# Performance work log

Hardware: AMD Instinct MI355X
Metric: run time of the kernel (lower is better)

## Reference

```python
import jax, jax.numpy as jnp
import numpy as np

N = 200000
B = 1024          # batch_size (number of graphs/segments)
D = 256           # in_channels
STEPS = 3         # processing_steps


def setup_inputs() -> dict:
    key = jax.random.key(0)
    ks = jax.random.split(key, 6)
    x = jax.random.normal(ks[0], (N, D), dtype=jnp.float32)
    bank_kg = jnp.zeros((1,), dtype=jnp.float32)  # unused by forward
    batch = jnp.sort(jax.random.randint(ks[1], (N,), 0, B, dtype=jnp.int32))
    q_star = jax.random.normal(ks[2], (B, 2 * D), dtype=jnp.float32)
    s = 1.0 / np.sqrt(D)  # PyTorch LSTM init scale
    W_ih = jax.random.uniform(ks[3], (4 * D, 2 * D), jnp.float32, -s, s)
    W_hh = jax.random.uniform(ks[4], (4 * D, D), jnp.float32, -s, s)
    b_ih = jnp.zeros((4 * D,), dtype=jnp.float32)
    b_hh = jnp.zeros((4 * D,), dtype=jnp.float32)
    return {"x": x, "bank_kg": bank_kg, "batch": batch, "q_star": q_star,
            "W_ih": W_ih, "W_hh": W_hh, "b_ih": b_ih, "b_hh": b_hh}


def _lstm_cell(inp, h, c, W_ih, W_hh, b_ih, b_hh):
    # PyTorch gate order: i, f, g, o
    gates = inp @ W_ih.T + b_ih + h @ W_hh.T + b_hh  # [B, 4D]
    i, f, g, o = jnp.split(gates, 4, axis=-1)
    i = jax.nn.sigmoid(i)
    f = jax.nn.sigmoid(f)
    g = jnp.tanh(g)
    o = jax.nn.sigmoid(o)
    c = f * c + i * g
    h = o * jnp.tanh(c)
    return h, c


def _segment_softmax(e, batch, num_segments):
    # numerically stable softmax over nodes grouped by segment id
    emax = jax.ops.segment_max(e, batch, num_segments=num_segments)
    emax = jnp.where(jnp.isfinite(emax), emax, 0.0)  # guard empty segments
    ee = jnp.exp(e - emax[batch])
    denom = jax.ops.segment_sum(ee, batch, num_segments=num_segments)
    return ee / (denom[batch] + 1e-16)


def reference(x, bank_kg, batch, q_star, W_ih, W_hh, b_ih, b_hh):
    del bank_kg  # unused in the original forward
    h = jnp.zeros((B, D), dtype=x.dtype)
    c = jnp.zeros((B, D), dtype=x.dtype)
    for _ in range(STEPS):
        h, c = _lstm_cell(q_star, h, c, W_ih, W_hh, b_ih, b_hh)
        q = h                                       # [B, D]
        e = jnp.sum(x * q[batch], axis=-1)          # [N] attention logits
        a = _segment_softmax(e, batch, B)           # [N]
        r = jax.ops.segment_sum(a[:, None] * x, batch, num_segments=B)  # [B, D]
        q_star = jnp.concatenate([q, r], axis=-1)   # [B, 2D]
    return q_star
```

## Files before the change

kernel.cpp:

```cpp
#include <hip/hip_runtime.h>
#include <hip/hip_bf16.h>
#include <cstdint>


#define NN     200000
#define BSEG   1024
#define DD     256
#define KA     512
#define FOURD  1024

using bf16x8 = __attribute__((ext_vector_type(8))) __bf16;
using f32x4  = __attribute__((ext_vector_type(4))) float;

__device__ __forceinline__ float bf2f(unsigned int u) {
  union { unsigned int i; float f; } v; v.i = (u & 0xffffu) << 16; return v.f;
}
__device__ __forceinline__ unsigned short f2bf(float f) {
  union { float f; unsigned int i; } v; v.f = f;
  unsigned int x = v.i;
  if ((x & 0x7fffffffu) > 0x7f800000u) return (unsigned short)((x >> 16) | 0x40);
  return (unsigned short)((x + 0x7fffu + ((x >> 16) & 1u)) >> 16);
}
__device__ __forceinline__ void split_bf(float f, unsigned short& hi, unsigned short& lo) {
  hi = f2bf(f);
  lo = f2bf(f - bf2f(hi));
}

__global__ void prep_all(const int* __restrict__ batch, int* __restrict__ segs,
                         const float* __restrict__ Wih, const float* __restrict__ Whh,
                         const float* __restrict__ bih, const float* __restrict__ bhh,
                         unsigned short* __restrict__ W1hi, unsigned short* __restrict__ W1lo,
                         unsigned short* __restrict__ W2hi, unsigned short* __restrict__ W2lo,
                         float* __restrict__ bias,
                         const float* __restrict__ qst,
                         unsigned short* __restrict__ Ahi, unsigned short* __restrict__ Alo,
                         float* __restrict__ c) {
  int idx = blockIdx.x * 256 + threadIdx.x;
  if (idx <= BSEG) {
    int lo = 0, hi = NN;
    while (lo < hi) { int mid = (lo + hi) >> 1; if (batch[mid] < idx) lo = mid + 1; else hi = mid; }
    segs[idx] = lo;
  }
  if (idx < FOURD) bias[idx] = bih[idx] + bhh[idx];
  if (idx < FOURD * KA) {
    int j = idx / KA, k = idx - j * KA;
    float w1 = Wih[j * 512 + k];
    float w2 = (k < 256) ? (Wih[j * 512 + k] + Whh[j * 256 + k])
                         : Wih[j * 512 + k];
    unsigned short hi, lo;
    split_bf(w1, hi, lo); W1hi[idx] = hi; W1lo[idx] = lo;
    split_bf(w2, hi, lo); W2hi[idx] = hi; W2lo[idx] = lo;
  }
  if (idx < BSEG * KA) {
    unsigned short hi, lo; split_bf(qst[idx], hi, lo);
    Ahi[idx] = hi; Alo[idx] = lo;
  }
  if (idx < BSEG * DD) c[idx] = 0.f;
}

__global__ __launch_bounds__(256) void gemm_gates(const unsigned short* __restrict__ Ahi,
                                                  const unsigned short* __restrict__ Alo,
                                                  const unsigned short* __restrict__ Whi,
                                                  const unsigned short* __restrict__ Wlo,
                                                  float* __restrict__ gates) {
  int bx = blockIdx.x;
  int m0 = (bx >> 5) << 7;
  int n0 = (bx & 31) << 5;
  int t = threadIdx.x, w = t >> 6, lane = t & 63;
  int r16 = lane & 15, quad = lane >> 4;

  __shared__ unsigned short sWhi[32 * 64];
  __shared__ unsigned short sWlo[32 * 64];

  f32x4 acc[2][2] = {};

  const unsigned short* a0h = Ahi + (size_t)(m0 + 32 * w + r16) * KA + quad * 8;
  const unsigned short* a0l = Alo + (size_t)(m0 + 32 * w + r16) * KA + quad * 8;

  int srow = t >> 3;
  int scb  = t & 7;
  const unsigned short* gwh = Whi + (size_t)(n0 + srow) * KA + scb * 8;
  const unsigned short* gwl = Wlo + (size_t)(n0 + srow) * KA + scb * 8;
  int sdst = srow * 64 + ((scb ^ (srow & 7)) * 8);

  for (int kc = 0; kc < KA; kc += 64) {
    __syncthreads();
    *(bf16x8*)&sWhi[sdst] = *(const bf16x8*)(gwh + kc);
    *(bf16x8*)&sWlo[sdst] = *(const bf16x8*)(gwl + kc);
    __syncthreads();
    #pragma unroll
    for (int ks = 0; ks < 2; ++ks) {
      bf16x8 bh[2], bl[2];
      #pragma unroll
      for (int ni = 0; ni < 2; ++ni) {
        int wr = 16 * ni + r16;
        int off = wr * 64 + (((ks * 4 + quad) ^ (wr & 7)) * 8);
        bh[ni] = *(const bf16x8*)&sWhi[off];
        bl[ni] = *(const bf16x8*)&sWlo[off];
      }
      #pragma unroll
      for (int ms = 0; ms < 2; ++ms) {
        bf16x8 a  = *(const bf16x8*)(a0h + (size_t)ms * 16 * KA + kc + ks * 32);
        bf16x8 al = *(const bf16x8*)(a0l + (size_t)ms * 16 * KA + kc + ks * 32);
        #pragma unroll
        for (int ni = 0; ni < 2; ++ni) {
          acc[ms][ni] = __builtin_amdgcn_mfma_f32_16x16x32_bf16(a,  bh[ni], acc[ms][ni], 0, 0, 0);
          acc[ms][ni] = __builtin_amdgcn_mfma_f32_16x16x32_bf16(a,  bl[ni], acc[ms][ni], 0, 0, 0);
          acc[ms][ni] = __builtin_amdgcn_mfma_f32_16x16x32_bf16(al, bh[ni], acc[ms][ni], 0, 0, 0);
        }
      }
    }
  }
  #pragma unroll
  for (int ms = 0; ms < 2; ++ms)
    #pragma unroll
    for (int ni = 0; ni < 2; ++ni)
      #pragma unroll
      for (int r = 0; r < 4; ++r)
        gates[(size_t)(m0 + 32 * w + 16 * ms + quad * 4 + r) * FOURD
              + n0 + 16 * ni + r16] = acc[ms][ni][r];
}

#define LD1(dst, kk, base, RR) do {                                         \
    int i_ = w + 4 * (kk);                                                  \
    int ic_ = i_ < (RR) ? i_ : (RR) - 1;                                    \
    if (ic_ < 0) ic_ = 0;                                                   \
    int row_ = (base) + ic_;                                                \
    if (row_ > NN - 1) row_ = NN - 1;                                       \
    dst = *(const float4*)(x + (size_t)row_ * DD + lane * 4);               \
  } while (0)

#define ST1(src, kk) do {                                                   \
    int i_ = w + 4 * (kk);                                                  \
    if (i_ < R) *(float4*)&xt[i_ * DD + ((4 * lane) ^ (4 * (i_ & 7)))] = src; \
  } while (0)

#define LDALL(base, RR) do {                                                \
    LD1(st0, 0, base, RR); LD1(st1, 1, base, RR);                           \
    LD1(st2, 2, base, RR); LD1(st3, 3, base, RR);                           \
    LD1(st4, 4, base, RR); LD1(st5, 5, base, RR);                           \
    LD1(st6, 6, base, RR); LD1(st7, 7, base, RR);                           \
  } while (0)

#define STALL() do {                                                        \
    ST1(st0, 0); ST1(st1, 1); ST1(st2, 2); ST1(st3, 3);                     \
    ST1(st4, 4); ST1(st5, 5); ST1(st6, 6); ST1(st7, 7);                     \
  } while (0)

__global__ __launch_bounds__(256, 4) void attn_fused(const float* __restrict__ x,
                                                     const int* __restrict__ segs,
                                                     const float* __restrict__ gates,
                                                     const float* __restrict__ bias,
                                                     float* __restrict__ c,
                                                     unsigned short* __restrict__ Ahi,
                                                     unsigned short* __restrict__ Alo,
                                                     float* __restrict__ qout) {
  int b = blockIdx.x, t = threadIdx.x;
  int w = t >> 6, lane = t & 63;

  const float* g = gates + (size_t)b * FOURD;
  float gi = g[t]       + bias[t];
  float gf = g[256 + t] + bias[256 + t];
  float gg = g[512 + t] + bias[512 + t];
  float go = g[768 + t] + bias[768 + t];
  float ig = 1.f / (1.f + expf(-gi));
  float fg = 1.f / (1.f + expf(-gf));
  float gt = tanhf(gg);
  float og = 1.f / (1.f + expf(-go));
  int cidx = b * DD + t;
  float cn = fg * c[cidx] + ig * gt;
  c[cidx] = cn;
  float hn = og * tanhf(cn);

  __shared__ float shq[DD];
  __shared__ __align__(16) float xt[32 * DD];
  __shared__ float se[32];
  __shared__ float sm[4], sl[4];
  __shared__ __align__(16) float sv[4][DD];

  shq[t ^ (4 * ((t >> 5) & 7))] = hn;
  {
    unsigned short hi, lo; split_bf(hn, hi, lo);
    size_t ro = (size_t)b * KA;
    Ahi[ro + t] = hi;  Alo[ro + t] = lo;
    qout[(size_t)b * 512 + t] = hn;
  }
  __syncthreads();

  int s = segs[b], e = segs[b + 1];
  int r8 = lane >> 3, d8 = lane & 7;

  float m = -3.402823466e38f, l = 0.f;
  float4 v = {0.f, 0.f, 0.f, 0.f};

  int R = e - s; if (R > 32) R = 32;
  float4 st0, st1, st2, st3, st4, st5, st6, st7;
  LDALL(s, R);

  for (int tb = s; tb < e; tb += 32) {
    __syncthreads();
    STALL();
    __syncthreads();

    int base2 = tb + 32;
    int Rn = e - base2; if (Rn > 32) Rn = 32;
    LDALL(base2, Rn);

    {
      int i = 8 * w + r8;
      int key = 4 * (i & 7);
      float4 acc = {0.f, 0.f, 0.f, 0.f};
      #pragma unroll
      for (int cc = 0; cc < 8; ++cc) {
        int j = d8 * 32 + 4 * cc;
        float4 xv = *(const float4*)&xt[i * DD + (j ^ key)];
        float4 qv = *(const float4*)&shq[j ^ (4 * d8)];
        acc.x += xv.x * qv.x; acc.y += xv.y * qv.y;
        acc.z += xv.z * qv.z; acc.w += xv.w * qv.w;
      }
      float ee = (acc.x + acc.y) + (acc.z + acc.w);
      ee += __shfl_xor(ee, 1);
      ee += __shfl_xor(ee, 2);
      ee += __shfl_xor(ee, 4);
      if (i >= R) ee = -3.402823466e38f;
      if (d8 == 0) se[i] = ee;
    }
    __syncthreads();

    float tm = se[lane & 31];
    #pragma unroll
    for (int mask = 16; mask; mask >>= 1) tm = fmaxf(tm, __shfl_xor(tm, mask));
    float mn = fmaxf(m, tm);
    float alpha = __expf(m - mn);
    l *= alpha; v.x *= alpha; v.y *= alpha; v.z *= alpha; v.w *= alpha;

    #pragma unroll
    for (int k = 0; k < 8; ++k) {
      int i = w + 4 * k;
      if (i < R) {
        float wv = __expf(se[i] - mn);
        float4 xv = *(const float4*)&xt[i * DD + ((4 * lane) ^ (4 * (i & 7)))];
        l += wv;
        v.x += wv * xv.x; v.y += wv * xv.y; v.z += wv * xv.z; v.w += wv * xv.w;
      }
    }
    m = mn;
    R = Rn;
  }

  if (lane == 0) { sm[w] = m; sl[w] = l; }
  *(float4*)(&sv[w][lane * 4]) = v;
  __syncthreads();

  float M = fmaxf(fmaxf(sm[0], sm[1]), fmaxf(sm[2], sm[3]));
  if (M < -1e37f) M = 0.f;
  float a0 = __expf(sm[0] - M), a1 = __expf(sm[1] - M);
  float a2 = __expf(sm[2] - M), a3 = __expf(sm[3] - M);
  float L = sl[0] * a0 + sl[1] * a1 + sl[2] * a2 + sl[3] * a3;
  float r = (sv[0][t] * a0 + sv[1][t] * a1 + sv[2][t] * a2 + sv[3][t] * a3)
            / (L + 1e-16f);

  unsigned short hi, lo; split_bf(r, hi, lo);
  size_t ro = (size_t)b * KA;
  Ahi[ro + DD + t] = hi;  Alo[ro + DD + t] = lo;
  qout[(size_t)b * 512 + DD + t] = r;
}

extern "C" void kernel_launch(void* const* d_in, const int* in_sizes, int n_in,
                              void* d_out, int out_size, void* d_ws, size_t ws_size,
                              hipStream_t stream) {
  const float* x    = (const float*)d_in[0];
  const int*   batc = (const int*)d_in[2];
  const float* qst  = (const float*)d_in[3];
  const float* Wih  = (const float*)d_in[4];
  const float* Whh  = (const float*)d_in[5];
  const float* bih  = (const float*)d_in[6];
  const float* bhh  = (const float*)d_in[7];
  float* out = (float*)d_out;

  char* ws = (char*)d_ws;
  size_t off = 0;
  auto alloc = [&](size_t bytes) -> void* {
    void* p = ws + off; off = (off + bytes + 255) & ~(size_t)255; return p;
  };
  int*            segs = (int*)alloc((size_t)(BSEG + 1) * 4);
  unsigned short* W1hi = (unsigned short*)alloc((size_t)FOURD * KA * 2);
  unsigned short* W1lo = (unsigned short*)alloc((size_t)FOURD * KA * 2);
  unsigned short* W2hi = (unsigned short*)alloc((size_t)FOURD * KA * 2);
  unsigned short* W2lo = (unsigned short*)alloc((size_t)FOURD * KA * 2);
  unsigned short* Ahi  = (unsigned short*)alloc((size_t)BSEG * KA * 2);
  unsigned short* Alo  = (unsigned short*)alloc((size_t)BSEG * KA * 2);
  float*          gate = (float*)alloc((size_t)BSEG * FOURD * 4);
  float*          c    = (float*)alloc((size_t)BSEG * DD * 4);
  float*          bias = (float*)alloc((size_t)FOURD * 4);

  prep_all<<<(FOURD * KA + 255) / 256, 256, 0, stream>>>(
      batc, segs, Wih, Whh, bih, bhh, W1hi, W1lo, W2hi, W2lo, bias, qst, Ahi, Alo, c);

  for (int step = 0; step < 3; ++step) {
    const unsigned short* whi = step ? W2hi : W1hi;
    const unsigned short* wlo = step ? W2lo : W1lo;
    gemm_gates<<<256, 256, 0, stream>>>(Ahi, Alo, whi, wlo, gate);
    attn_fused<<<BSEG, 256, 0, stream>>>(x, segs, gate, bias, c, Ahi, Alo, out);
  }
}
```

Measured before the change: 428.9 us.

## Fuse prep, gate GEMM and attention into one persistent kernel with grid barriers

Replaces the prep kernel and the three gemm/attention launch pairs with a single 1024-block kernel that synchronises steps through a software grid barrier built on atomics. The LSTM cell state now stays in a register across steps, and the gate GEMM becomes a per-block 32x32 tile that reads operands directly from global memory with no LDS staging. The intent is to remove launch overhead and the round trips of c and bias through memory. In exchange, it requires all 1024 blocks to be co-resident (launch_bounds of 4 blocks per CU), which risks deadlock or spin overhead, and the GEMM loses its LDS reuse of the weights.

New measurement: 1.568 ms. 266% more time.

```diff
diff --git a/kernel.cpp b/kernel.cpp
--- a/kernel.cpp
+++ b/kernel.cpp
@@ -8,6 +8,7 @@
 #define DD     256
 #define KA     512
 #define FOURD  1024
+#define NBLK   1024
 
 using bf16x8 = __attribute__((ext_vector_type(8))) __bf16;
 using f32x4  = __attribute__((ext_vector_type(4))) float;
@@ -26,99 +27,24 @@
   lo = f2bf(f - bf2f(hi));
 }
 
-__global__ void prep_all(const int* __restrict__ batch, int* __restrict__ segs,
-                         const float* __restrict__ Wih, const float* __restrict__ Whh,
-                         const float* __restrict__ bih, const float* __restrict__ bhh,
-                         unsigned short* __restrict__ W1hi, unsigned short* __restrict__ W1lo,
-                         unsigned short* __restrict__ W2hi, unsigned short* __restrict__ W2lo,
-                         float* __restrict__ bias,
-                         const float* __restrict__ qst,
-                         unsigned short* __restrict__ Ahi, unsigned short* __restrict__ Alo,
-                         float* __restrict__ c) {
-  int idx = blockIdx.x * 256 + threadIdx.x;
-  if (idx <= BSEG) {
-    int lo = 0, hi = NN;
-    while (lo < hi) { int mid = (lo + hi) >> 1; if (batch[mid] < idx) lo = mid + 1; else hi = mid; }
-    segs[idx] = lo;
-  }
-  if (idx < FOURD) bias[idx] = bih[idx] + bhh[idx];
-  if (idx < FOURD * KA) {
-    int j = idx / KA, k = idx - j * KA;
-    float w1 = Wih[j * 512 + k];
-    float w2 = (k < 256) ? (Wih[j * 512 + k] + Whh[j * 256 + k])
-                         : Wih[j * 512 + k];
-    unsigned short hi, lo;
-    split_bf(w1, hi, lo); W1hi[idx] = hi; W1lo[idx] = lo;
-    split_bf(w2, hi, lo); W2hi[idx] = hi; W2lo[idx] = lo;
-  }
-  if (idx < BSEG * KA) {
-    unsigned short hi, lo; split_bf(qst[idx], hi, lo);
-    Ahi[idx] = hi; Alo[idx] = lo;
-  }
-  if (idx < BSEG * DD) c[idx] = 0.f;
-}
-
-__global__ __launch_bounds__(256) void gemm_gates(const unsigned short* __restrict__ Ahi,
-                                                  const unsigned short* __restrict__ Alo,
-                                                  const unsigned short* __restrict__ Whi,
-                                                  const unsigned short* __restrict__ Wlo,
-                                                  float* __restrict__ gates) {
-  int bx = blockIdx.x;
-  int m0 = (bx >> 5) << 7;
-  int n0 = (bx & 31) << 5;
-  int t = threadIdx.x, w = t >> 6, lane = t & 63;
-  int r16 = lane & 15, quad = lane >> 4;
-
-  __shared__ unsigned short sWhi[32 * 64];
-  __shared__ unsigned short sWlo[32 * 64];
-
-  f32x4 acc[2][2] = {};
-
-  const unsigned short* a0h = Ahi + (size_t)(m0 + 32 * w + r16) * KA + quad * 8;
-  const unsigned short* a0l = Alo + (size_t)(m0 + 32 * w + r16) * KA + quad * 8;
-
-  int srow = t >> 3;
-  int scb  = t & 7;
-  const unsigned short* gwh = Whi + (size_t)(n0 + srow) * KA + scb * 8;
-  const unsigned short* gwl = Wlo + (size_t)(n0 + srow) * KA + scb * 8;
-  int sdst = srow * 64 + ((scb ^ (srow & 7)) * 8);
-
-  for (int kc = 0; kc < KA; kc += 64) {
-    __syncthreads();
-    *(bf16x8*)&sWhi[sdst] = *(const bf16x8*)(gwh + kc);
-    *(bf16x8*)&sWlo[sdst] = *(const bf16x8*)(gwl + kc);
-    __syncthreads();
-    #pragma unroll
-    for (int ks = 0; ks < 2; ++ks) {
-      bf16x8 bh[2], bl[2];
-      #pragma unroll
-      for (int ni = 0; ni < 2; ++ni) {
-        int wr = 16 * ni + r16;
-        int off = wr * 64 + (((ks * 4 + quad) ^ (wr & 7)) * 8);
-        bh[ni] = *(const bf16x8*)&sWhi[off];
-        bl[ni] = *(const bf16x8*)&sWlo[off];
-      }
-      #pragma unroll
-      for (int ms = 0; ms < 2; ++ms) {
-        bf16x8 a  = *(const bf16x8*)(a0h + (size_t)ms * 16 * KA + kc + ks * 32);
-        bf16x8 al = *(const bf16x8*)(a0l + (size_t)ms * 16 * KA + kc + ks * 32);
-        #pragma unroll
-        for (int ni = 0; ni < 2; ++ni) {
-          acc[ms][ni] = __builtin_amdgcn_mfma_f32_16x16x32_bf16(a,  bh[ni], acc[ms][ni], 0, 0, 0);
-          acc[ms][ni] = __builtin_amdgcn_mfma_f32_16x16x32_bf16(a,  bl[ni], acc[ms][ni], 0, 0, 0);
-          acc[ms][ni] = __builtin_amdgcn_mfma_f32_16x16x32_bf16(al, bh[ni], acc[ms][ni], 0, 0, 0);
-        }
-      }
-    }
-  }
-  #pragma unroll
-  for (int ms = 0; ms < 2; ++ms)
-    #pragma unroll
-    for (int ni = 0; ni < 2; ++ni)
-      #pragma unroll
-      for (int r = 0; r < 4; ++r)
-        gates[(size_t)(m0 + 32 * w + 16 * ms + quad * 4 + r) * FOURD
-              + n0 + 16 * ni + r16] = acc[ms][ni][r];
+__device__ __forceinline__ void grid_barrier(int* bar, int& gen) {
+  __syncthreads();
+  if (threadIdx.x == 0) {
+    __threadfence();
+    gen++;
+    int prev = __hip_atomic_fetch_add(&bar[0], 1, __ATOMIC_ACQ_REL,
+                                      __HIP_MEMORY_SCOPE_AGENT);
+    if (prev == NBLK - 1) {
+      __hip_atomic_store(&bar[0], 0, __ATOMIC_RELAXED, __HIP_MEMORY_SCOPE_AGENT);
+      __hip_atomic_fetch_add(&bar[1], 1, __ATOMIC_RELEASE,
+                             __HIP_MEMORY_SCOPE_AGENT);
+    } else {
+      while (__hip_atomic_load(&bar[1], __ATOMIC_ACQUIRE,
+                               __HIP_MEMORY_SCOPE_AGENT) < gen)
+        __builtin_amdgcn_s_sleep(2);
+    }
+  }
+  __syncthreads();
 }
 
 #define LD1(dst, kk, base, RR) do {                                         \
@@ -147,123 +73,194 @@
     ST1(st4, 4); ST1(st5, 5); ST1(st6, 6); ST1(st7, 7);                     \
   } while (0)
 
-__global__ __launch_bounds__(256, 4) void attn_fused(const float* __restrict__ x,
-                                                     const int* __restrict__ segs,
-                                                     const float* __restrict__ gates,
-                                                     const float* __restrict__ bias,
-                                                     float* __restrict__ c,
-                                                     unsigned short* __restrict__ Ahi,
-                                                     unsigned short* __restrict__ Alo,
-                                                     float* __restrict__ qout) {
+__global__ __launch_bounds__(256, 4) void set2set_all(
+    const float* __restrict__ x, const int* __restrict__ batch,
+    const float* __restrict__ qst, const float* __restrict__ Wih,
+    const float* __restrict__ Whh, const float* __restrict__ bih,
+    const float* __restrict__ bhh,
+    int* __restrict__ segs,
+    unsigned short* __restrict__ W1hi, unsigned short* __restrict__ W1lo,
+    unsigned short* __restrict__ W2hi, unsigned short* __restrict__ W2lo,
+    unsigned short* __restrict__ Ahi, unsigned short* __restrict__ Alo,
+    float* __restrict__ gates, int* __restrict__ bar,
+    float* __restrict__ qout) {
   int b = blockIdx.x, t = threadIdx.x;
   int w = t >> 6, lane = t & 63;
-
-  const float* g = gates + (size_t)b * FOURD;
-  float gi = g[t]       + bias[t];
-  float gf = g[256 + t] + bias[256 + t];
-  float gg = g[512 + t] + bias[512 + t];
-  float go = g[768 + t] + bias[768 + t];
-  float ig = 1.f / (1.f + expf(-gi));
-  float fg = 1.f / (1.f + expf(-gf));
-  float gt = tanhf(gg);
-  float og = 1.f / (1.f + expf(-go));
-  int cidx = b * DD + t;
-  float cn = fg * c[cidx] + ig * gt;
-  c[cidx] = cn;
-  float hn = og * tanhf(cn);
+  int r16 = lane & 15, quad = lane >> 4;
+  int gen = 0;
+
+  #pragma unroll
+  for (int rep = 0; rep < 2; ++rep) {
+    int idx = b * 256 + t + rep * 262144;
+    int j = idx >> 9, kk = idx & 511;
+    float w1 = Wih[idx];
+    float w2 = (kk < 256) ? w1 + Whh[j * 256 + kk] : w1;
+    unsigned short hi, lo;
+    split_bf(w1, hi, lo); W1hi[idx] = hi; W1lo[idx] = lo;
+    split_bf(w2, hi, lo); W2hi[idx] = hi; W2lo[idx] = lo;
+    float a = qst[idx];
+    split_bf(a, hi, lo); Ahi[idx] = hi; Alo[idx] = lo;
+  }
+  {
+    int gidx = b * 256 + t;
+    if (gidx <= BSEG) {
+      int lo = 0, hi = NN;
+      while (lo < hi) { int mid = (lo + hi) >> 1; if (batch[mid] < gidx) lo = mid + 1; else hi = mid; }
+      segs[gidx] = lo;
+    }
+  }
+  float bi0 = bih[t]       + bhh[t];
+  float bi1 = bih[256 + t] + bhh[256 + t];
+  float bi2 = bih[512 + t] + bhh[512 + t];
+  float bi3 = bih[768 + t] + bhh[768 + t];
+
+  grid_barrier(bar, gen);
+
+  int s0 = segs[b], e0 = segs[b + 1];
+
+  int m0 = (b >> 5) << 5;
+  int n0 = (b & 31) << 5;
+  int arow = m0 + ((w >> 1) << 4) + r16;
+  int bcol = n0 + ((w & 1) << 4) + r16;
 
   __shared__ float shq[DD];
   __shared__ __align__(16) float xt[32 * DD];
   __shared__ float se[32];
-  __shared__ float sm[4], sl[4];
+  __shared__ float smw[4], slw[4];
   __shared__ __align__(16) float sv[4][DD];
 
-  shq[t ^ (4 * ((t >> 5) & 7))] = hn;
-  {
-    unsigned short hi, lo; split_bf(hn, hi, lo);
+  float cc = 0.f;
+
+  for (int step = 0; step < 3; ++step) {
+    const unsigned short* Whi_ = step ? W2hi : W1hi;
+    const unsigned short* Wlo_ = step ? W2lo : W1lo;
+
+    {
+      const unsigned short* ah  = Ahi  + (size_t)arow * KA + quad * 8;
+      const unsigned short* al  = Alo  + (size_t)arow * KA + quad * 8;
+      const unsigned short* bhp = Whi_ + (size_t)bcol * KA + quad * 8;
+      const unsigned short* blp = Wlo_ + (size_t)bcol * KA + quad * 8;
+      f32x4 acc = {};
+      #pragma unroll 4
+      for (int kk = 0; kk < 16; ++kk) {
+        bf16x8 a  = *(const bf16x8*)(ah  + kk * 32);
+        bf16x8 aL = *(const bf16x8*)(al  + kk * 32);
+        bf16x8 bh = *(const bf16x8*)(bhp + kk * 32);
+        bf16x8 bl = *(const bf16x8*)(blp + kk * 32);
+        acc = __builtin_amdgcn_mfma_f32_16x16x32_bf16(a,  bh, acc, 0, 0, 0);
+        acc = __builtin_amdgcn_mfma_f32_16x16x32_bf16(a,  bl, acc, 0, 0, 0);
+        acc = __builtin_amdgcn_mfma_f32_16x16x32_bf16(aL, bh, acc, 0, 0, 0);
+      }
+      int orow = m0 + ((w >> 1) << 4) + quad * 4;
+      int ocol = n0 + ((w & 1) << 4) + r16;
+      #pragma unroll
+      for (int r = 0; r < 4; ++r)
+        gates[(size_t)(orow + r) * FOURD + ocol] = acc[r];
+    }
+    grid_barrier(bar, gen);
+
+    const float* g = gates + (size_t)b * FOURD;
+    float gi = g[t]       + bi0;
+    float gf = g[256 + t] + bi1;
+    float gg = g[512 + t] + bi2;
+    float go = g[768 + t] + bi3;
+    float ig = 1.f / (1.f + expf(-gi));
+    float fg = 1.f / (1.f + expf(-gf));
+    float gt = tanhf(gg);
+    float og = 1.f / (1.f + expf(-go));
+    float cn = fg * cc + ig * gt;
+    cc = cn;
+    float hn = og * tanhf(cn);
+
+    shq[t ^ (4 * ((t >> 5) & 7))] = hn;
+    {
+      unsigned short hi, lo; split_bf(hn, hi, lo);
+      size_t ro = (size_t)b * KA;
+      Ahi[ro + t] = hi;  Alo[ro + t] = lo;
+      qout[(size_t)b * 512 + t] = hn;
+    }
+    __syncthreads();
+
+    int s = s0, e = e0;
+    int r8 = lane >> 3, d8 = lane & 7;
+
+    float m = -3.402823466e38f, l = 0.f;
+    float4 v = {0.f, 0.f, 0.f, 0.f};
+
+    int R = e - s; if (R > 32) R = 32;
+    float4 st0, st1, st2, st3, st4, st5, st6, st7;
+    LDALL(s, R);
+
+    for (int tb = s; tb < e; tb += 32) {
+      __syncthreads();
+      STALL();
+      __syncthreads();
+
+      int base2 = tb + 32;
+      int Rn = e - base2; if (Rn > 32) Rn = 32;
+      LDALL(base2, Rn);
+
+      {
+        int i = 8 * w + r8;
+        int key = 4 * (i & 7);
+        float4 acc = {0.f, 0.f, 0.f, 0.f};
+        #pragma unroll
+        for (int ccn = 0; ccn < 8; ++ccn) {
+          int jj = d8 * 32 + 4 * ccn;
+          float4 xv = *(const float4*)&xt[i * DD + (jj ^ key)];
+          float4 qv = *(const float4*)&shq[jj ^ (4 * d8)];
+          acc.x += xv.x * qv.x; acc.y += xv.y * qv.y;
+          acc.z += xv.z * qv.z; acc.w += xv.w * qv.w;
+        }
+        float ee = (acc.x + acc.y) + (acc.z + acc.w);
+        ee += __shfl_xor(ee, 1);
+        ee += __shfl_xor(ee, 2);
+        ee += __shfl_xor(ee, 4);
+        if (i >= R) ee = -3.402823466e38f;
+        if (d8 == 0) se[i] = ee;
+      }
+      __syncthreads();
+
+      float tm = se[lane & 31];
+      #pragma unroll
+      for (int mask = 16; mask; mask >>= 1) tm = fmaxf(tm, __shfl_xor(tm, mask));
+      float mn = fmaxf(m, tm);
+      float alpha = __expf(m - mn);
+      l *= alpha; v.x *= alpha; v.y *= alpha; v.z *= alpha; v.w *= alpha;
+
+      #pragma unroll
+      for (int k = 0; k < 8; ++k) {
+        int i = w + 4 * k;
+        if (i < R) {
+          float wv = __expf(se[i] - mn);
+          float4 xv = *(const float4*)&xt[i * DD + ((4 * lane) ^ (4 * (i & 7)))];
+          l += wv;
+          v.x += wv * xv.x; v.y += wv * xv.y; v.z += wv * xv.z; v.w += wv * xv.w;
+        }
+      }
+      m = mn;
+      R = Rn;
+    }
+
+    if (lane == 0) { smw[w] = m; slw[w] = l; }
+    *(float4*)(&sv[w][lane * 4]) = v;
+    __syncthreads();
+
+    float M = fmaxf(fmaxf(smw[0], smw[1]), fmaxf(smw[2], smw[3]));
+    if (M < -1e37f) M = 0.f;
+    float a0 = __expf(smw[0] - M), a1 = __expf(smw[1] - M);
+    float a2 = __expf(smw[2] - M), a3 = __expf(smw[3] - M);
+    float L = slw[0] * a0 + slw[1] * a1 + slw[2] * a2 + slw[3] * a3;
+    float r = (sv[0][t] * a0 + sv[1][t] * a1 + sv[2][t] * a2 + sv[3][t] * a3)
+              / (L + 1e-16f);
+
+    unsigned short hi, lo; split_bf(r, hi, lo);
     size_t ro = (size_t)b * KA;
-    Ahi[ro + t] = hi;  Alo[ro + t] = lo;
-    qout[(size_t)b * 512 + t] = hn;
-  }
-  __syncthreads();
-
-  int s = segs[b], e = segs[b + 1];
-  int r8 = lane >> 3, d8 = lane & 7;
-
-  float m = -3.402823466e38f, l = 0.f;
-  float4 v = {0.f, 0.f, 0.f, 0.f};
-
-  int R = e - s; if (R > 32) R = 32;
-  float4 st0, st1, st2, st3, st4, st5, st6, st7;
-  LDALL(s, R);
-
-  for (int tb = s; tb < e; tb += 32) {
-    __syncthreads();
-    STALL();
-    __syncthreads();
-
-    int base2 = tb + 32;
-    int Rn = e - base2; if (Rn > 32) Rn = 32;
-    LDALL(base2, Rn);
-
-    {
-      int i = 8 * w + r8;
-      int key = 4 * (i & 7);
-      float4 acc = {0.f, 0.f, 0.f, 0.f};
-      #pragma unroll
-      for (int cc = 0; cc < 8; ++cc) {
-        int j = d8 * 32 + 4 * cc;
-        float4 xv = *(const float4*)&xt[i * DD + (j ^ key)];
-        float4 qv = *(const float4*)&shq[j ^ (4 * d8)];
-        acc.x += xv.x * qv.x; acc.y += xv.y * qv.y;
-        acc.z += xv.z * qv.z; acc.w += xv.w * qv.w;
-      }
-      float ee = (acc.x + acc.y) + (acc.z + acc.w);
-      ee += __shfl_xor(ee, 1);
-      ee += __shfl_xor(ee, 2);
-      ee += __shfl_xor(ee, 4);
-      if (i >= R) ee = -3.402823466e38f;
-      if (d8 == 0) se[i] = ee;
-    }
-    __syncthreads();
-
-    float tm = se[lane & 31];
-    #pragma unroll
-    for (int mask = 16; mask; mask >>= 1) tm = fmaxf(tm, __shfl_xor(tm, mask));
-    float mn = fmaxf(m, tm);
-    float alpha = __expf(m - mn);
-    l *= alpha; v.x *= alpha; v.y *= alpha; v.z *= alpha; v.w *= alpha;
-
-    #pragma unroll
-    for (int k = 0; k < 8; ++k) {
-      int i = w + 4 * k;
-      if (i < R) {
-        float wv = __expf(se[i] - mn);
-        float4 xv = *(const float4*)&xt[i * DD + ((4 * lane) ^ (4 * (i & 7)))];
-        l += wv;
-        v.x += wv * xv.x; v.y += wv * xv.y; v.z += wv * xv.z; v.w += wv * xv.w;
-      }
-    }
-    m = mn;
-    R = Rn;
-  }
-
-  if (lane == 0) { sm[w] = m; sl[w] = l; }
-  *(float4*)(&sv[w][lane * 4]) = v;
-  __syncthreads();
-
-  float M = fmaxf(fmaxf(sm[0], sm[1]), fmaxf(sm[2], sm[3]));
-  if (M < -1e37f) M = 0.f;
-  float a0 = __expf(sm[0] - M), a1 = __expf(sm[1] - M);
-  float a2 = __expf(sm[2] - M), a3 = __expf(sm[3] - M);
-  float L = sl[0] * a0 + sl[1] * a1 + sl[2] * a2 + sl[3] * a3;
-  float r = (sv[0][t] * a0 + sv[1][t] * a1 + sv[2][t] * a2 + sv[3][t] * a3)
-            / (L + 1e-16f);
-
-  unsigned short hi, lo; split_bf(r, hi, lo);
-  size_t ro = (size_t)b * KA;
-  Ahi[ro + DD + t] = hi;  Alo[ro + DD + t] = lo;
-  qout[(size_t)b * 512 + DD + t] = r;
+    Ahi[ro + DD + t] = hi;  Alo[ro + DD + t] = lo;
+    qout[(size_t)b * 512 + DD + t] = r;
+
+    if (step < 2) grid_barrier(bar, gen);
+  }
 }
 
 extern "C" void kernel_launch(void* const* d_in, const int* in_sizes, int n_in,
@@ -283,6 +280,7 @@
   auto alloc = [&](size_t bytes) -> void* {
     void* p = ws + off; off = (off + bytes + 255) & ~(size_t)255; return p;
   };
+  int*            bar  = (int*)alloc(256);
   int*            segs = (int*)alloc((size_t)(BSEG + 1) * 4);
   unsigned short* W1hi = (unsigned short*)alloc((size_t)FOURD * KA * 2);
   unsigned short* W1lo = (unsigned short*)alloc((size_t)FOURD * KA * 2);
@@ -291,16 +289,9 @@
   unsigned short* Ahi  = (unsigned short*)alloc((size_t)BSEG * KA * 2);
   unsigned short* Alo  = (unsigned short*)alloc((size_t)BSEG * KA * 2);
   float*          gate = (float*)alloc((size_t)BSEG * FOURD * 4);
-  float*          c    = (float*)alloc((size_t)BSEG * DD * 4);
-  float*          bias = (float*)alloc((size_t)FOURD * 4);
-
-  prep_all<<<(FOURD * KA + 255) / 256, 256, 0, stream>>>(
-      batc, segs, Wih, Whh, bih, bhh, W1hi, W1lo, W2hi, W2lo, bias, qst, Ahi, Alo, c);
-
-  for (int step = 0; step < 3; ++step) {
-    const unsigned short* whi = step ? W2hi : W1hi;
-    const unsigned short* wlo = step ? W2lo : W1lo;
-    gemm_gates<<<256, 256, 0, stream>>>(Ahi, Alo, whi, wlo, gate);
-    attn_fused<<<BSEG, 256, 0, stream>>>(x, segs, gate, bias, c, Ahi, Alo, out);
-  }
-}
+
+  hipMemsetAsync(bar, 0, 2 * sizeof(int), stream);
+  set2set_all<<<NBLK, 256, 0, stream>>>(
+      x, batc, qst, Wih, Whh, bih, bhh,
+      segs, W1hi, W1lo, W2hi, W2lo, Ahi, Alo, gate, bar, out);
+}
```
